# Optimization experiments

Measured on AMD Instinct MI355X. Metric: run time of the kernel, lower is better.

The kernel has to match this reference:

```python
import jax, jax.numpy as jnp
import numpy as np

HID = 1024
NH = 16
HD = 64
INTER = 2816
EPS = 1e-5


def _rms_norm(x, eps=EPS):
    x32 = x.astype(jnp.float32)
    var = jnp.mean(x32 * x32, axis=-1, keepdims=True)
    return (x32 * jax.lax.rsqrt(var + eps)).astype(x.dtype)


def _rotate_half(x):
    x1, x2 = jnp.split(x, 2, axis=-1)
    return jnp.concatenate([-x2, x1], axis=-1)


def setup_inputs() -> dict:
    key = jax.random.key(0)
    ks = jax.random.split(key, 6)
    B, S = 1, 2048
    # real RoPE tables: [S, HD]
    inv_freq = 1.0 / (10000.0 ** (np.arange(0, HD, 2, dtype=np.float32) / HD))
    t = np.arange(S, dtype=np.float32)
    freqs = np.outer(t, inv_freq)  # [S, HD/2]
    emb = np.concatenate([freqs, freqs], axis=-1)  # [S, HD]
    cos = jnp.asarray(np.cos(emb))
    sin = jnp.asarray(np.sin(emb))
    sc = 0.02
    return {
        "cos": cos,
        "sin": sin,
        "hidden_states": jax.random.normal(ks[0], (B, S, HID), jnp.float32),
        "attn_bias": jax.random.normal(ks[1], (B, NH, S, S), jnp.float32) * 0.1,
        "w_qkv": jax.random.normal(ks[2], (HID, (NH + 2 * NH) * HD), jnp.float32) * sc,
        "w_o": jax.random.normal(ks[3], (NH * HD, HID), jnp.float32) * sc,
        "w_gate_up": jax.random.normal(ks[4], (HID, 2 * INTER), jnp.float32) * sc,
        "w_down": jax.random.normal(ks[5], (INTER, HID), jnp.float32) * sc,
    }


def _attention(cos, sin, x, attn_bias, w_qkv, w_o):
    B, S, _ = x.shape
    qkv = (x @ w_qkv).reshape(B, S, 3 * NH, HD)
    q = qkv[:, :, :NH]          # [B,S,H,D]
    k = qkv[:, :, NH:2 * NH]
    v = qkv[:, :, 2 * NH:]
    c = cos[None, :, None, :]
    s = sin[None, :, None, :]
    q = q * c + _rotate_half(q) * s
    k = k * c + _rotate_half(k) * s
    scale = HD ** -0.5
    scores = jnp.einsum('bqhd,bkhd->bhqk', q, k) * scale + attn_bias
    attn = jax.nn.softmax(scores.astype(jnp.float32), axis=-1).astype(q.dtype)
    out = jnp.einsum('bhqk,bkhd->bqhd', attn, v).reshape(B, S, NH * HD)
    return out @ w_o


def _swiglu(x, w_gate_up, w_down):
    gu = x @ w_gate_up
    gate, up = jnp.split(gu, 2, axis=-1)
    return (jax.nn.silu(gate) * up) @ w_down


def reference(cos, sin, hidden_states, attn_bias, w_qkv, w_o, w_gate_up, w_down):
    x = hidden_states
    x = _rms_norm(x + _attention(cos, sin, x, attn_bias, w_qkv, w_o))
    x = _rms_norm(x + _swiglu(x, w_gate_up, w_down))
    return x
```

## Files before the change

### kernel.cpp

```cpp
#include <hip/hip_runtime.h>
#include <stdint.h>

using u16 = unsigned short;
typedef __bf16 bf16x8 __attribute__((ext_vector_type(8)));
typedef float f32x4 __attribute__((ext_vector_type(4)));

__device__ __forceinline__ u16 f2bf(float f) {
  union { float f; uint32_t u; } v; v.f = f;
  uint32_t r = v.u + 0x7fffu + ((v.u >> 16) & 1u);
  return (u16)(r >> 16);
}
__device__ __forceinline__ float bf2f(u16 h) {
  union { uint32_t u; float f; } v; v.u = ((uint32_t)h) << 16;
  return v.f;
}
__device__ __forceinline__ bf16x8 ldb8(const u16* p) {
  return *reinterpret_cast<const bf16x8*>(p);
}
__device__ __forceinline__ void gload_lds16(const void* g, void* l) {
  __builtin_amdgcn_global_load_lds(
      (const __attribute__((address_space(1))) void*)g,
      (__attribute__((address_space(3))) void*)l, 16, 0, 0);
}

__global__ __launch_bounds__(256) void prep_kernel(
    const float* __restrict__ w_qkv, const float* __restrict__ w_o,
    const float* __restrict__ w_gu, const float* __restrict__ w_down,
    const float* __restrict__ hidden, u16* __restrict__ wqkv_t,
    u16* __restrict__ wo_t, u16* __restrict__ wgu_t, u16* __restrict__ wd_t,
    u16* __restrict__ xb) {
  const int b = blockIdx.x;
  const int t = threadIdx.x;

  if (b >= 12544) {
    int idx = (b - 12544) * 256 + t;
    float4 v = *(const float4*)(hidden + (size_t)idx * 4);
    ushort4 o;
    o.x = f2bf(v.x); o.y = f2bf(v.y); o.z = f2bf(v.z); o.w = f2bf(v.w);
    *(ushort4*)(xb + (size_t)idx * 4) = o;
    return;
  }

  const float* W;
  u16* Wt;
  int N, K, lb;
  bool perm = false;
  if (b < 3072)      { W = w_qkv; Wt = wqkv_t; N = 3072; K = 1024; lb = b; }
  else if (b < 4096) { W = w_o;   Wt = wo_t;   N = 1024; K = 1024; lb = b - 3072; }
  else if (b < 9728) { W = w_gu;  Wt = wgu_t;  N = 5632; K = 1024; lb = b - 4096; perm = true; }
  else               { W = w_down; Wt = wd_t;  N = 1024; K = 2816; lb = b - 9728; }

  const int nx = N >> 5;
  const int n0 = (lb % nx) * 32, k0 = (lb / nx) * 32;
  const int tx = t & 31, ty = t >> 5;

  __shared__ u16 tile[32][33];
  const int nc = n0 + tx;
  const int src_col = perm ? (((nc & 1) == 0) ? (nc >> 1) : 2816 + (nc >> 1))
                           : nc;
#pragma unroll
  for (int i = 0; i < 32; i += 8)
    tile[ty + i][tx] = f2bf(W[(size_t)(k0 + ty + i) * N + src_col]);
  __syncthreads();
#pragma unroll
  for (int i = 0; i < 32; i += 8)
    Wt[(size_t)(n0 + ty + i) * K + k0 + tx] = tile[tx][ty + i];
}

__global__ __launch_bounds__(256) void gemm_qkv_rope(
    const u16* __restrict__ A, const u16* __restrict__ Bt,
    const float* __restrict__ cosb, const float* __restrict__ sinb,
    u16* __restrict__ qb, u16* __restrict__ kb, u16* __restrict__ vt,
    int M, int N, int K) {
  __shared__ __align__(16) u16 As[2][128 * 32];
  __shared__ __align__(16) u16 Bs[2][128 * 32];
  __shared__ u16 vbuf[4][64][17];
  const int tid = threadIdx.x;
  const int w = tid >> 6, lane = tid & 63;
  const int wr = w >> 1, wc = w & 1;
  const int r16 = lane & 15, g = lane >> 4;
  const int nwg = gridDim.x * gridDim.y;
  const int idx = blockIdx.y * gridDim.x + blockIdx.x;
  const int swz = (idx & 7) * (nwg >> 3) + (idx >> 3);
  const int m0 = (swz / gridDim.x) * 128, n0 = (swz % gridDim.x) * 128;
  const int ldrow = lane >> 2;
  const int ldk = (lane & 3) * 8;
  const int NT = K >> 5;

  f32x4 acc[4][4] = {};

#define STG_QKV(tt, b_)                                                   \
  do {                                                                    \
    const int kt_ = (tt) * 32;                                            \
    _Pragma("unroll") for (int i = 0; i < 2; ++i) {                       \
      int chunk = w * 2 + i;                                              \
      int row = chunk * 16 + ldrow;                                       \
      gload_lds16(A + (size_t)(m0 + row) * K + kt_ + ldk,                 \
                  &As[b_][chunk * 512]);                                  \
      gload_lds16(Bt + (size_t)(n0 + row) * K + kt_ + ldk,                \
                  &Bs[b_][chunk * 512]);                                  \
    }                                                                     \
  } while (0)

  STG_QKV(0, 0);
  asm volatile("s_waitcnt vmcnt(0)" ::: "memory");
  __builtin_amdgcn_s_barrier();

  int cur = 0;
  for (int t = 0; t < NT; ++t) {
    if (t + 1 < NT) STG_QKV(t + 1, cur ^ 1);
    bf16x8 a[4], b[4];
#pragma unroll
    for (int mt = 0; mt < 4; ++mt)
      a[mt] = ldb8(&As[cur][(wr * 64 + mt * 16 + r16) * 32 + g * 8]);
#pragma unroll
    for (int nt = 0; nt < 4; ++nt)
      b[nt] = ldb8(&Bs[cur][(wc * 64 + nt * 16 + r16) * 32 + g * 8]);
#pragma unroll
    for (int mt = 0; mt < 4; ++mt)
#pragma unroll
      for (int nt = 0; nt < 4; ++nt)
        acc[mt][nt] = __builtin_amdgcn_mfma_f32_16x16x32_bf16(
            a[mt], b[nt], acc[mt][nt], 0, 0, 0);
    asm volatile("s_waitcnt vmcnt(0) lgkmcnt(0)" ::: "memory");
    __builtin_amdgcn_s_barrier();
    cur ^= 1;
  }

  const int type = n0 >> 10;
  const int head = ((n0 & 1023) >> 6) + wc;
  if (type < 2) {
    u16* outp = type == 0 ? qb : kb;
    const float qs = type == 0 ? 0.125f : 1.0f;
#pragma unroll
    for (int mt = 0; mt < 4; ++mt)
#pragma unroll
      for (int r = 0; r < 4; ++r) {
        const int srow = m0 + wr * 64 + mt * 16 + g * 4 + r;
#pragma unroll
        for (int nt = 0; nt < 4; ++nt) {
          const int d = nt * 16 + r16;
          float cv = cosb[srow * 64 + d];
          float sv = sinb[srow * 64 + d];
          float sgn = nt < 2 ? -1.f : 1.f;
          float val = acc[mt][nt][r] * cv + sgn * acc[mt][nt ^ 2][r] * sv;
          outp[((size_t)head * 2048 + srow) * 64 + d] = f2bf(val * qs);
        }
      }
  } else {
    const int s_base = m0 + wr * 64;
    const int dl = lane >> 2;
    const int sblk = (lane & 3) * 16;
#pragma unroll
    for (int nt = 0; nt < 4; ++nt) {
#pragma unroll
      for (int mt = 0; mt < 4; ++mt)
#pragma unroll
        for (int r = 0; r < 4; ++r)
          vbuf[w][mt * 16 + g * 4 + r][r16] = f2bf(acc[mt][nt][r]);
      u16* dst =
          vt + ((size_t)(head * 64 + nt * 16 + dl)) * 2048 + s_base + sblk;
#pragma unroll
      for (int jj = 0; jj < 4; ++jj) {
        ushort4 ov;
        ov.x = vbuf[w][sblk + jj * 4 + 0][dl];
        ov.y = vbuf[w][sblk + jj * 4 + 1][dl];
        ov.z = vbuf[w][sblk + jj * 4 + 2][dl];
        ov.w = vbuf[w][sblk + jj * 4 + 3][dl];
        *(ushort4*)(dst + jj * 4) = ov;
      }
    }
  }
}

__global__ __launch_bounds__(256) void gemm_bt_swiglu(
    const u16* __restrict__ A, const u16* __restrict__ Bt,
    u16* __restrict__ Hb, int M, int N, int K) {
  __shared__ __align__(16) u16 As[2][128 * 32];
  __shared__ __align__(16) u16 Bs[2][128 * 32];
  const int tid = threadIdx.x;
  const int w = tid >> 6, lane = tid & 63;
  const int wr = w >> 1, wc = w & 1;
  const int r16 = lane & 15, g = lane >> 4;
  const int nwg = gridDim.x * gridDim.y;
  const int idx = blockIdx.y * gridDim.x + blockIdx.x;
  const int swz = (idx & 7) * (nwg >> 3) + (idx >> 3);
  const int m0 = (swz / gridDim.x) * 128, n0 = (swz % gridDim.x) * 128;
  const int ldrow = lane >> 2;
  const int ldk = (lane & 3) * 8;
  const int NT = K >> 5;

  f32x4 acc[4][4] = {};

  STG_QKV(0, 0);
  asm volatile("s_waitcnt vmcnt(0)" ::: "memory");
  __builtin_amdgcn_s_barrier();

  int cur = 0;
  for (int t = 0; t < NT; ++t) {
    if (t + 1 < NT) STG_QKV(t + 1, cur ^ 1);
    bf16x8 a[4], b[4];
#pragma unroll
    for (int mt = 0; mt < 4; ++mt)
      a[mt] = ldb8(&As[cur][(wr * 64 + mt * 16 + r16) * 32 + g * 8]);
#pragma unroll
    for (int nt = 0; nt < 4; ++nt)
      b[nt] = ldb8(&Bs[cur][(wc * 64 + nt * 16 + r16) * 32 + g * 8]);
#pragma unroll
    for (int mt = 0; mt < 4; ++mt)
#pragma unroll
      for (int nt = 0; nt < 4; ++nt)
        acc[mt][nt] = __builtin_amdgcn_mfma_f32_16x16x32_bf16(
            a[mt], b[nt], acc[mt][nt], 0, 0, 0);
    asm volatile("s_waitcnt vmcnt(0) lgkmcnt(0)" ::: "memory");
    __builtin_amdgcn_s_barrier();
    cur ^= 1;
  }
#pragma unroll
  for (int mt = 0; mt < 4; ++mt)
#pragma unroll
    for (int nt = 0; nt < 4; ++nt)
#pragma unroll
      for (int r = 0; r < 4; ++r) {
        float val = acc[mt][nt][r];
        float other = __shfl_xor(val, 1);
        if ((r16 & 1) == 0) {
          float o = val / (1.f + __expf(-val)) * other;
          int row = m0 + wr * 64 + mt * 16 + g * 4 + r;
          int col = n0 + wc * 64 + nt * 16 + r16;
          Hb[(size_t)row * 2816 + (col >> 1)] = f2bf(o);
        }
      }
}

__global__ __launch_bounds__(256) void gemm_bt6464(
    const u16* __restrict__ A, const u16* __restrict__ Bt,
    u16* __restrict__ C, int M, int N, int K) {
  __shared__ __align__(16) u16 As[2][64 * 32];
  __shared__ __align__(16) u16 Bs[2][64 * 32];
  const int tid = threadIdx.x;
  const int w = tid >> 6, lane = tid & 63;
  const int wr = w >> 1, wc = w & 1;
  const int r16 = lane & 15, g = lane >> 4;
  const int nwg = gridDim.x * gridDim.y;
  const int idx = blockIdx.y * gridDim.x + blockIdx.x;
  const int swz = (idx & 7) * (nwg >> 3) + (idx >> 3);
  const int m0 = (swz / gridDim.x) * 64, n0 = (swz % gridDim.x) * 64;
  const int ldrow = lane >> 2;
  const int ldk = (lane & 3) * 8;
  const int NT = K >> 5;

  f32x4 acc[2][2] = {};

#define STG_6464(tt, b_)                                                  \
  do {                                                                    \
    const int kt_ = (tt) * 32;                                            \
    _Pragma("unroll") for (int i = 0; i < 2; ++i) {                       \
      int chunk = w * 2 + i;                                              \
      if (chunk < 4) {                                                    \
        int row = chunk * 16 + ldrow;                                     \
        gload_lds16(A + (size_t)(m0 + row) * K + kt_ + ldk,               \
                    &As[b_][chunk * 512]);                                \
      } else {                                                            \
        int cb = chunk - 4;                                               \
        int row = cb * 16 + ldrow;                                        \
        gload_lds16(Bt + (size_t)(n0 + row) * K + kt_ + ldk,              \
                    &Bs[b_][cb * 512]);                                   \
      }                                                                   \
    }                                                                     \
  } while (0)

  STG_6464(0, 0);
  asm volatile("s_waitcnt vmcnt(0)" ::: "memory");
  __builtin_amdgcn_s_barrier();

  int cur = 0;
  for (int t = 0; t < NT; ++t) {
    if (t + 1 < NT) STG_6464(t + 1, cur ^ 1);
    bf16x8 a[2], b[2];
#pragma unroll
    for (int mt = 0; mt < 2; ++mt)
      a[mt] = ldb8(&As[cur][(wr * 32 + mt * 16 + r16) * 32 + g * 8]);
#pragma unroll
    for (int nt = 0; nt < 2; ++nt)
      b[nt] = ldb8(&Bs[cur][(wc * 32 + nt * 16 + r16) * 32 + g * 8]);
#pragma unroll
    for (int mt = 0; mt < 2; ++mt)
#pragma unroll
      for (int nt = 0; nt < 2; ++nt)
        acc[mt][nt] = __builtin_amdgcn_mfma_f32_16x16x32_bf16(
            a[mt], b[nt], acc[mt][nt], 0, 0, 0);
    asm volatile("s_waitcnt vmcnt(0) lgkmcnt(0)" ::: "memory");
    __builtin_amdgcn_s_barrier();
    cur ^= 1;
  }
#pragma unroll
  for (int mt = 0; mt < 2; ++mt)
#pragma unroll
    for (int nt = 0; nt < 2; ++nt)
#pragma unroll
      for (int r = 0; r < 4; ++r) {
        int row = m0 + wr * 32 + mt * 16 + g * 4 + r;
        int col = n0 + wc * 32 + nt * 16 + r16;
        C[(size_t)row * N + col] = f2bf(acc[mt][nt][r]);
      }
}

__global__ __launch_bounds__(256, 2) void attn_kernel(
    const u16* __restrict__ qb, const u16* __restrict__ kb,
    const u16* __restrict__ vt, const float* __restrict__ bias,
    u16* __restrict__ attnb) {
  const int bid = blockIdx.x;
  const int swz = (bid & 7) * 64 + (bid >> 3);
  const int h = swz >> 5;
  const int qt = swz & 31;
  const int tid = threadIdx.x;
  const int w = tid >> 6;
  const int lane = tid & 63;
  const int r16 = lane & 15, g = lane >> 4;

  __shared__ __align__(16) u16 P_lds[4][16 * 40];
  __shared__ float acc_s[4][16][64];
  __shared__ float m_s[4][16], l_s[4][16];

  bf16x8 qf0[4], qf1[4];
#pragma unroll
  for (int st = 0; st < 4; ++st) {
    const u16* qrow =
        qb + ((size_t)h * 2048 + qt * 64 + st * 16 + r16) * 64;
    qf0[st] = ldb8(qrow + g * 8);
    qf1[st] = ldb8(qrow + 32 + g * 8);
  }

  f32x4 acc[4][4] = {};
  float m[4], lsum[4];
#pragma unroll
  for (int st = 0; st < 4; ++st) { m[st] = -1e30f; lsum[st] = 0.f; }

  const float* bbase = bias + ((size_t)h * 2048 + qt * 64) * 2048;

  const int kv0 = w * 512, kv1 = kv0 + 512;
  for (int kt = kv0; kt < kv1; kt += 32) {
    bf16x8 ka[2], kc[2];
#pragma unroll
    for (int c = 0; c < 2; ++c) {
      const u16* krow = kb + ((size_t)h * 2048 + kt + c * 16 + r16) * 64;
      ka[c] = ldb8(krow + g * 8);
      kc[c] = ldb8(krow + 32 + g * 8);
    }
    bf16x8 vf[4];
#pragma unroll
    for (int nt = 0; nt < 4; ++nt)
      vf[nt] =
          ldb8(vt + ((size_t)h * 64 + nt * 16 + r16) * 2048 + kt + g * 8);
    float4 bv[4][2];
#pragma unroll
    for (int st = 0; st < 4; ++st) {
      bv[st][0] = *(const float4*)(bbase +
          (size_t)(st * 16 + r16) * 2048 + kt + g * 4);
      bv[st][1] = *(const float4*)(bbase +
          (size_t)(st * 16 + r16) * 2048 + kt + 16 + g * 4);
    }

#pragma unroll
    for (int st = 0; st < 4; ++st) {
      f32x4 sc[2];
#pragma unroll
      for (int c = 0; c < 2; ++c) {
        f32x4 z = {0.f, 0.f, 0.f, 0.f};
        f32x4 t =
            __builtin_amdgcn_mfma_f32_16x16x32_bf16(ka[c], qf0[st], z, 0, 0, 0);
        sc[c] =
            __builtin_amdgcn_mfma_f32_16x16x32_bf16(kc[c], qf1[st], t, 0, 0, 0);
      }
      sc[0][0] += bv[st][0].x; sc[0][1] += bv[st][0].y;
      sc[0][2] += bv[st][0].z; sc[0][3] += bv[st][0].w;
      sc[1][0] += bv[st][1].x; sc[1][1] += bv[st][1].y;
      sc[1][2] += bv[st][1].z; sc[1][3] += bv[st][1].w;

      float t8 = fmaxf(fmaxf(fmaxf(sc[0][0], sc[0][1]), fmaxf(sc[0][2], sc[0][3])),
                       fmaxf(fmaxf(sc[1][0], sc[1][1]), fmaxf(sc[1][2], sc[1][3])));
      t8 = fmaxf(t8, __shfl_xor(t8, 16));
      t8 = fmaxf(t8, __shfl_xor(t8, 32));
      float mnew = fmaxf(m[st], t8);
      float alpha = __expf(m[st] - mnew);
      m[st] = mnew;

      float ps = 0.f;
#pragma unroll
      for (int c = 0; c < 2; ++c)
#pragma unroll
        for (int r = 0; r < 4; ++r) {
          float p = __expf(sc[c][r] - mnew);
          sc[c][r] = p;
          ps += p;
        }
      lsum[st] = lsum[st] * alpha + ps;

      float av[4];
#pragma unroll
      for (int r = 0; r < 4; ++r) av[r] = __shfl(alpha, g * 4 + r);
#pragma unroll
      for (int nt = 0; nt < 4; ++nt)
#pragma unroll
        for (int r = 0; r < 4; ++r) acc[st][nt][r] *= av[r];

#pragma unroll
      for (int c = 0; c < 2; ++c)
#pragma unroll
        for (int r = 0; r < 4; ++r)
          P_lds[w][r16 * 40 + c * 16 + g * 4 + r] = f2bf(sc[c][r]);
      bf16x8 pf = ldb8(&P_lds[w][r16 * 40 + g * 8]);
#pragma unroll
      for (int nt = 0; nt < 4; ++nt)
        acc[st][nt] = __builtin_amdgcn_mfma_f32_16x16x32_bf16(
            pf, vf[nt], acc[st][nt], 0, 0, 0);
    }
  }

#pragma unroll
  for (int st = 0; st < 4; ++st) {
    __syncthreads();
#pragma unroll
    for (int nt = 0; nt < 4; ++nt)
#pragma unroll
      for (int r = 0; r < 4; ++r)
        acc_s[w][g * 4 + r][nt * 16 + r16] = acc[st][nt][r];
    {
      float t = lsum[st];
      t += __shfl_xor(t, 16);
      t += __shfl_xor(t, 32);
      if (lane < 16) {
        l_s[w][r16] = t;
        m_s[w][r16] = m[st];
      }
    }
    __syncthreads();

    const int row = tid >> 4;
    const int col4 = (tid & 15) * 4;
    float m0v = m_s[0][row], m1v = m_s[1][row], m2v = m_s[2][row],
          m3v = m_s[3][row];
    float mm = fmaxf(fmaxf(m0v, m1v), fmaxf(m2v, m3v));
    float s0 = __expf(m0v - mm), s1 = __expf(m1v - mm);
    float s2 = __expf(m2v - mm), s3 = __expf(m3v - mm);
    float ltot = l_s[0][row] * s0 + l_s[1][row] * s1 + l_s[2][row] * s2 +
                 l_s[3][row] * s3;
    float inv = 1.f / ltot;
    ushort4 ov;
    u16* outp =
        attnb + (size_t)(qt * 64 + st * 16 + row) * 1024 + h * 64 + col4;
#pragma unroll
    for (int j = 0; j < 4; ++j) {
      float v = acc_s[0][row][col4 + j] * s0 + acc_s[1][row][col4 + j] * s1 +
                acc_s[2][row][col4 + j] * s2 + acc_s[3][row][col4 + j] * s3;
      ((u16*)&ov)[j] = f2bf(v * inv);
    }
    *(ushort4*)outp = ov;
  }
}

__global__ __launch_bounds__(256) void addnorm_kernel(
    const float* __restrict__ resid, const u16* __restrict__ delta,
    float* __restrict__ outf, u16* __restrict__ outb) {
  int row = blockIdx.x, tid = threadIdx.x;
  size_t base = (size_t)row * 1024 + tid * 4;
  float4 rv = *(const float4*)(resid + base);
  ushort4 dv = *(const ushort4*)(delta + base);
  float x0 = rv.x + bf2f(dv.x);
  float x1 = rv.y + bf2f(dv.y);
  float x2 = rv.z + bf2f(dv.z);
  float x3 = rv.w + bf2f(dv.w);
  float ss = x0 * x0 + x1 * x1 + x2 * x2 + x3 * x3;
#pragma unroll
  for (int sh = 32; sh >= 1; sh >>= 1) ss += __shfl_xor(ss, sh);
  __shared__ float red[4];
  if ((tid & 63) == 0) red[tid >> 6] = ss;
  __syncthreads();
  float tot = red[0] + red[1] + red[2] + red[3];
  float rstd = rsqrtf(tot * (1.0f / 1024.0f) + 1e-5f);
  float4 ov;
  ov.x = x0 * rstd; ov.y = x1 * rstd; ov.z = x2 * rstd; ov.w = x3 * rstd;
  *(float4*)(outf + base) = ov;
  if (outb) {
    ushort4 ob;
    ob.x = f2bf(ov.x); ob.y = f2bf(ov.y); ob.z = f2bf(ov.z); ob.w = f2bf(ov.w);
    *(ushort4*)(outb + base) = ob;
  }
}

extern "C" void kernel_launch(void* const* d_in, const int* in_sizes, int n_in,
                              void* d_out, int out_size, void* d_ws,
                              size_t ws_size, hipStream_t stream) {
  (void)in_sizes; (void)n_in; (void)out_size; (void)ws_size;
  const float* cosb  = (const float*)d_in[0];
  const float* sinb  = (const float*)d_in[1];
  const float* hidden = (const float*)d_in[2];
  const float* bias  = (const float*)d_in[3];
  const float* w_qkv = (const float*)d_in[4];
  const float* w_o   = (const float*)d_in[5];
  const float* w_gu  = (const float*)d_in[6];
  const float* w_down = (const float*)d_in[7];
  float* out = (float*)d_out;

  char* p = (char*)d_ws;
  auto alloc = [&](size_t bytes) {
    void* r = (void*)p;
    p += (bytes + 255) & ~(size_t)255;
    return r;
  };
  u16* wqkv_t = (u16*)alloc((size_t)3072 * 1024 * 2);
  u16* wo_t   = (u16*)alloc((size_t)1024 * 1024 * 2);
  u16* wgu_t  = (u16*)alloc((size_t)5632 * 1024 * 2);
  u16* wd_t   = (u16*)alloc((size_t)1024 * 2816 * 2);
  u16* xb     = (u16*)alloc((size_t)2048 * 1024 * 2);
  u16* qb     = (u16*)alloc((size_t)16 * 2048 * 64 * 2);
  u16* kb     = (u16*)alloc((size_t)16 * 2048 * 64 * 2);
  u16* vt     = (u16*)alloc((size_t)16 * 2048 * 64 * 2);
  u16* attnb  = (u16*)alloc((size_t)2048 * 1024 * 2);
  u16* ob     = (u16*)alloc((size_t)2048 * 1024 * 2);
  float* x1f  = (float*)alloc((size_t)2048 * 1024 * 4);
  u16* x1b    = (u16*)alloc((size_t)2048 * 1024 * 2);
  u16* hb     = (u16*)alloc((size_t)2048 * 2816 * 2);
  u16* mlpb   = (u16*)alloc((size_t)2048 * 1024 * 2);

  prep_kernel<<<14592, 256, 0, stream>>>(w_qkv, w_o, w_gu, w_down, hidden,
                                         wqkv_t, wo_t, wgu_t, wd_t, xb);

  gemm_qkv_rope<<<dim3(3072 / 128, 2048 / 128), 256, 0, stream>>>(
      xb, wqkv_t, cosb, sinb, qb, kb, vt, 2048, 3072, 1024);
  attn_kernel<<<512, 256, 0, stream>>>(qb, kb, vt, bias, attnb);
  gemm_bt6464<<<dim3(1024 / 64, 2048 / 64), 256, 0, stream>>>(attnb, wo_t, ob, 2048, 1024, 1024);
  addnorm_kernel<<<2048, 256, 0, stream>>>(hidden, ob, x1f, x1b);
  gemm_bt_swiglu<<<dim3(5632 / 128, 2048 / 128), 256, 0, stream>>>(x1b, wgu_t, hb, 2048, 5632, 1024);
  gemm_bt6464<<<dim3(1024 / 64, 2048 / 64), 256, 0, stream>>>(hb, wd_t, mlpb, 2048, 1024, 2816);
  addnorm_kernel<<<2048, 256, 0, stream>>>(x1f, mlpb, out, nullptr);
}
```

Before: 241.5 us.

## Split attention KV range across eight waves per block instead of four

The attention kernel now launches 512 threads per block. Each of eight waves processes 256 keys instead of 512, and the final cross-wave softmax merge combines eight partial states. This gives each query tile more parallelism and shorter serial KV loops, which suits the small grid of 512 blocks on a large GPU. In exchange, shared memory for the partial accumulators doubles, the reduction does more work, and 512-thread blocks with launch bounds of 2 per CU may force register limits.

```diff
diff --git a/kernel.cpp b/kernel.cpp
--- a/kernel.cpp
+++ b/kernel.cpp
@@ -306,7 +306,7 @@
       }
 }
 
-__global__ __launch_bounds__(256, 2) void attn_kernel(
+__global__ __launch_bounds__(512, 2) void attn_kernel(
     const u16* __restrict__ qb, const u16* __restrict__ kb,
     const u16* __restrict__ vt, const float* __restrict__ bias,
     u16* __restrict__ attnb) {
@@ -319,9 +319,9 @@
   const int lane = tid & 63;
   const int r16 = lane & 15, g = lane >> 4;
 
-  __shared__ __align__(16) u16 P_lds[4][16 * 40];
-  __shared__ float acc_s[4][16][64];
-  __shared__ float m_s[4][16], l_s[4][16];
+  __shared__ __align__(16) u16 P_lds[8][16 * 40];
+  __shared__ float acc_s[8][16][64];
+  __shared__ float m_s[8][16], l_s[8][16];
 
   bf16x8 qf0[4], qf1[4];
 #pragma unroll
@@ -339,7 +339,7 @@
 
   const float* bbase = bias + ((size_t)h * 2048 + qt * 64) * 2048;
 
-  const int kv0 = w * 512, kv1 = kv0 + 512;
+  const int kv0 = w * 256, kv1 = kv0 + 256;
   for (int kt = kv0; kt < kv1; kt += 32) {
     bf16x8 ka[2], kc[2];
 #pragma unroll
@@ -437,26 +437,30 @@
     }
     __syncthreads();
 
-    const int row = tid >> 4;
-    const int col4 = (tid & 15) * 4;
-    float m0v = m_s[0][row], m1v = m_s[1][row], m2v = m_s[2][row],
-          m3v = m_s[3][row];
-    float mm = fmaxf(fmaxf(m0v, m1v), fmaxf(m2v, m3v));
-    float s0 = __expf(m0v - mm), s1 = __expf(m1v - mm);
-    float s2 = __expf(m2v - mm), s3 = __expf(m3v - mm);
-    float ltot = l_s[0][row] * s0 + l_s[1][row] * s1 + l_s[2][row] * s2 +
-                 l_s[3][row] * s3;
+    const int row = tid >> 5;
+    const int col2 = (tid & 31) * 2;
+    float mm = m_s[0][row];
+#pragma unroll
+    for (int w8 = 1; w8 < 8; ++w8) mm = fmaxf(mm, m_s[w8][row]);
+    float sw[8];
+    float ltot = 0.f;
+#pragma unroll
+    for (int w8 = 0; w8 < 8; ++w8) {
+      sw[w8] = __expf(m_s[w8][row] - mm);
+      ltot += l_s[w8][row] * sw[w8];
+    }
     float inv = 1.f / ltot;
-    ushort4 ov;
-    u16* outp =
-        attnb + (size_t)(qt * 64 + st * 16 + row) * 1024 + h * 64 + col4;
-#pragma unroll
-    for (int j = 0; j < 4; ++j) {
-      float v = acc_s[0][row][col4 + j] * s0 + acc_s[1][row][col4 + j] * s1 +
-                acc_s[2][row][col4 + j] * s2 + acc_s[3][row][col4 + j] * s3;
-      ((u16*)&ov)[j] = f2bf(v * inv);
-    }
-    *(ushort4*)outp = ov;
+    float v0 = 0.f, v1 = 0.f;
+#pragma unroll
+    for (int w8 = 0; w8 < 8; ++w8) {
+      v0 += acc_s[w8][row][col2] * sw[w8];
+      v1 += acc_s[w8][row][col2 + 1] * sw[w8];
+    }
+    ushort2 ov;
+    ov.x = f2bf(v0 * inv);
+    ov.y = f2bf(v1 * inv);
+    *(ushort2*)(attnb + (size_t)(qt * 64 + st * 16 + row) * 1024 + h * 64 +
+                col2) = ov;
   }
 }
 
@@ -529,7 +533,7 @@
 
   gemm_qkv_rope<<<dim3(3072 / 128, 2048 / 128), 256, 0, stream>>>(
       xb, wqkv_t, cosb, sinb, qb, kb, vt, 2048, 3072, 1024);
-  attn_kernel<<<512, 256, 0, stream>>>(qb, kb, vt, bias, attnb);
+  attn_kernel<<<512, 512, 0, stream>>>(qb, kb, vt, bias, attnb);
   gemm_bt6464<<<dim3(1024 / 64, 2048 / 64), 256, 0, stream>>>(attnb, wo_t, ob, 2048, 1024, 1024);
   addnorm_kernel<<<2048, 256, 0, stream>>>(hidden, ob, x1f, x1b);
   gemm_bt_swiglu<<<dim3(5632 / 128, 2048 / 128), 256, 0, stream>>>(x1b, wgu_t, hb, 2048, 5632, 1024);
```

Result: slower. 246.6 us (+2.1%).
